# Performance work log

Measured on AMD Instinct MI355X. Metric: run time of the kernel, lower is better.

Reference implementation:

```python
import jax, jax.numpy as jnp
import numpy as np

B, L, D, H = 8, 1024, 512, 8
HD = D // H            # head_dim = 64
MAX_SEQ = 1024         # max_sequence_len
TEMP = 1.0


def setup_inputs() -> dict:
    key = jax.random.key(0)
    ks = jax.random.split(key, 9)
    w = lambda k, shape: jax.random.normal(k, shape, jnp.float32) * 0.02
    return {
        "x_q": jax.random.normal(ks[0], (B, L, D), jnp.float32),
        "x_k": jax.random.normal(ks[1], (B, L, D), jnp.float32),
        "x_v": jax.random.normal(ks[2], (B, L, D), jnp.float32),
        # causal mask: 1 where future (masked), 0 elsewhere; added as mask * -1e9
        "mask": jnp.triu(jnp.ones((L, L), jnp.float32), k=1),
        "Wq": w(ks[3], (D, D)), "bq": jnp.zeros((D,), jnp.float32),
        "Wk": w(ks[4], (D, D)), "bk": jnp.zeros((D,), jnp.float32),
        "Wv": w(ks[5], (D, D)), "bv": jnp.zeros((D,), jnp.float32),
        "Wo": w(ks[6], (D, D)), "bo": jnp.zeros((D,), jnp.float32),
        "rel_emb": w(ks[7], (MAX_SEQ, HD)),
    }


def _heads(x, W, b):
    # Dense + split heads: [B,L,D] -> [B,H,L,HD]
    y = x @ W + b
    Bx, Lx, _ = x.shape
    return y.reshape(Bx, Lx, H, HD).transpose(0, 2, 1, 3)


def reference(x_q, x_k, x_v, mask, Wq, bq, Wk, bk, Wv, bv, Wo, bo, rel_emb):
    Bx, Lq, Dx = x_q.shape
    Lk = x_k.shape[1]
    q = _heads(x_q, Wq, bq)   # [B,H,Lq,HD]
    k = _heads(x_k, Wk, bk)   # [B,H,Lk,HD]
    v = _heads(x_v, Wv, bv)   # [B,H,Lk,HD]

    scores = jnp.einsum('bhld,bhmd->bhlm', q, k)  # [B,H,Lq,Lk]

    # relative-position scores (Music Transformer skew trick)
    start = max(0, MAX_SEQ - Lq)
    E = rel_emb[start:]                              # [M,HD], M == Lq
    M = E.shape[0]
    rel = jnp.einsum('bhld,md->bhlm', q, E)          # [B,H,Lq,M]
    rel_mask = jnp.flip(jnp.tril(jnp.ones((Lq, M), jnp.float32)), axis=1)
    rel = rel * rel_mask
    # skew: pad one col on left, reshape swapping last two dims, drop first row
    padded = jnp.pad(rel, ((0, 0), (0, 0), (0, 0), (1, 0)))       # [B,H,Lq,M+1]
    skewed = padded.reshape(Bx, H, M + 1, Lq)[:, :, 1:, :]        # [B,H,M,Lq]
    skewed = skewed[:, :, :, :Lk]                                 # key_len <= query_len

    logits = (scores + skewed) / (jnp.sqrt(jnp.float32(HD)) * TEMP)
    logits = logits + mask * (-1e9)
    attn = jax.nn.softmax(logits, axis=-1)                        # [B,H,Lq,Lk]

    out = jnp.einsum('bhlm,bhmd->bhld', attn, v)                  # [B,H,Lq,HD]
    out = out.transpose(0, 2, 1, 3).reshape(Bx, Lq, Dx)
    out = out @ Wo + bo
    return out, attn
```

## Files before the change

### kernel.cpp

```cpp
#include <hip/hip_runtime.h>

typedef unsigned short u16;
typedef short bf8 __attribute__((ext_vector_type(8)));
typedef float f32x4 __attribute__((ext_vector_type(4)));

#define Bc 8
#define Hc 8
#define Lc 1024
#define Dc 512
#define HDc 64

__device__ __forceinline__ u16 f2bf(float f) {
    unsigned int x; __builtin_memcpy(&x, &f, 4);
    x = x + 0x7fffu + ((x >> 16) & 1u);
    return (u16)(x >> 16);
}
union S8 { bf8 v; u16 s[8]; };

__global__ __launch_bounds__(256) void relcvt(const float* __restrict__ src,
                                              u16* __restrict__ dst) {
    const int idx = blockIdx.x * 256 + threadIdx.x;
    const float4 v = *(const float4*)(src + (size_t)idx * 4);
    ushort4 o; o.x = f2bf(v.x); o.y = f2bf(v.y); o.z = f2bf(v.z); o.w = f2bf(v.w);
    *(ushort4*)(dst + (size_t)idx * 4) = o;
}

__global__ __launch_bounds__(256) void wtrans(
    const float* __restrict__ w0, const float* __restrict__ w1,
    const float* __restrict__ w2, const float* __restrict__ w3,
    u16* __restrict__ o0, u16* __restrict__ o1,
    u16* __restrict__ o2, u16* __restrict__ o3)
{
    const float* W; u16* O;
    switch (blockIdx.z) {
        case 0: W = w0; O = o0; break;
        case 1: W = w1; O = o1; break;
        case 2: W = w2; O = o2; break;
        default: W = w3; O = o3; break;
    }
    __shared__ float tile[64][65];
    const int t = threadIdx.x;
    const int k0 = blockIdx.x * 64, n0 = blockIdx.y * 64;
#pragma unroll
    for (int s = 0; s < 4; ++s) {
        const int idx = s * 256 + t;
        const int r = idx >> 4, c = (idx & 15) * 4;
        const float4 v = *(const float4*)(W + (size_t)(k0 + r) * Dc + n0 + c);
        tile[r][c] = v.x; tile[r][c + 1] = v.y; tile[r][c + 2] = v.z; tile[r][c + 3] = v.w;
    }
    __syncthreads();
#pragma unroll
    for (int s = 0; s < 2; ++s) {
        const int idx = s * 256 + t;
        const int rn = idx >> 3, ck = (idx & 7) * 8;
        S8 o;
#pragma unroll
        for (int u = 0; u < 8; ++u) o.s[u] = f2bf(tile[ck + u][rn]);
        *(bf8*)(O + (size_t)(n0 + rn) * Dc + k0 + ck) = o.v;
    }
}

__global__ __launch_bounds__(256) void gemm_mfma(
    const void* __restrict__ A, const u16* __restrict__ WT,
    const float* __restrict__ bias, void* __restrict__ Y,
    int aF32, int mode)
{
    __shared__ u16 As[2][64][72];
    __shared__ u16 Bs[2][64][72];

    const int wgid = blockIdx.x;
    const int xcd = wgid & 7, rr = wgid >> 3;
    const int mt = xcd + 8 * (rr >> 3), ntile = rr & 7;
    const int m0 = mt * 64, n0 = ntile * 64;

    const int t = threadIdx.x;
    const int w = t >> 6, lane = t & 63, quad = lane >> 4, l15 = lane & 15;
    const int ra = t >> 2, ca = (t & 3) * 16;

    f32x4 acc[4] = {};

    {
        S8 o0, o1;
        if (aF32) {
            const float* ap = (const float*)A + (size_t)(m0 + ra) * Dc + ca;
            const float4 v0 = *(const float4*)ap,       v1 = *(const float4*)(ap + 4);
            const float4 v2 = *(const float4*)(ap + 8), v3 = *(const float4*)(ap + 12);
            o0.s[0] = f2bf(v0.x); o0.s[1] = f2bf(v0.y); o0.s[2] = f2bf(v0.z); o0.s[3] = f2bf(v0.w);
            o0.s[4] = f2bf(v1.x); o0.s[5] = f2bf(v1.y); o0.s[6] = f2bf(v1.z); o0.s[7] = f2bf(v1.w);
            o1.s[0] = f2bf(v2.x); o1.s[1] = f2bf(v2.y); o1.s[2] = f2bf(v2.z); o1.s[3] = f2bf(v2.w);
            o1.s[4] = f2bf(v3.x); o1.s[5] = f2bf(v3.y); o1.s[6] = f2bf(v3.z); o1.s[7] = f2bf(v3.w);
        } else {
            const u16* ap = (const u16*)A + (size_t)(m0 + ra) * Dc + ca;
            o0.v = *(const bf8*)ap; o1.v = *(const bf8*)(ap + 8);
        }
        *(bf8*)&As[0][ra][ca] = o0.v; *(bf8*)&As[0][ra][ca + 8] = o1.v;
        const u16* bp = WT + (size_t)(n0 + ra) * Dc + ca;
        *(bf8*)&Bs[0][ra][ca] = *(const bf8*)bp;
        *(bf8*)&Bs[0][ra][ca + 8] = *(const bf8*)(bp + 8);
    }

    int cur = 0;
    for (int k0 = 0; k0 < Dc; k0 += 64) {
        __syncthreads();
        const bool pf = (k0 + 64 < Dc);
        float4 v0, v1, v2, v3; bf8 an0 = {}, an1 = {}, bn0 = {}, bn1 = {};
        if (pf) {
            const int kn = k0 + 64;
            if (aF32) {
                const float* ap = (const float*)A + (size_t)(m0 + ra) * Dc + kn + ca;
                v0 = *(const float4*)ap;       v1 = *(const float4*)(ap + 4);
                v2 = *(const float4*)(ap + 8); v3 = *(const float4*)(ap + 12);
            } else {
                const u16* ap = (const u16*)A + (size_t)(m0 + ra) * Dc + kn + ca;
                an0 = *(const bf8*)ap; an1 = *(const bf8*)(ap + 8);
            }
            const u16* bp = WT + (size_t)(n0 + ra) * Dc + kn + ca;
            bn0 = *(const bf8*)bp; bn1 = *(const bf8*)(bp + 8);
        }

#pragma unroll
        for (int ks = 0; ks < 2; ++ks) {
            const bf8 a = *(const bf8*)&As[cur][w * 16 + l15][ks * 32 + quad * 8];
#pragma unroll
            for (int nt = 0; nt < 4; ++nt) {
                const bf8 b = *(const bf8*)&Bs[cur][nt * 16 + l15][ks * 32 + quad * 8];
                acc[nt] = __builtin_amdgcn_mfma_f32_16x16x32_bf16(a, b, acc[nt], 0, 0, 0);
            }
        }

        if (pf) {
            S8 o0, o1;
            if (aF32) {
                o0.s[0] = f2bf(v0.x); o0.s[1] = f2bf(v0.y); o0.s[2] = f2bf(v0.z); o0.s[3] = f2bf(v0.w);
                o0.s[4] = f2bf(v1.x); o0.s[5] = f2bf(v1.y); o0.s[6] = f2bf(v1.z); o0.s[7] = f2bf(v1.w);
                o1.s[0] = f2bf(v2.x); o1.s[1] = f2bf(v2.y); o1.s[2] = f2bf(v2.z); o1.s[3] = f2bf(v2.w);
                o1.s[4] = f2bf(v3.x); o1.s[5] = f2bf(v3.y); o1.s[6] = f2bf(v3.z); o1.s[7] = f2bf(v3.w);
            } else { o0.v = an0; o1.v = an1; }
            *(bf8*)&As[cur ^ 1][ra][ca] = o0.v; *(bf8*)&As[cur ^ 1][ra][ca + 8] = o1.v;
            *(bf8*)&Bs[cur ^ 1][ra][ca] = bn0;  *(bf8*)&Bs[cur ^ 1][ra][ca + 8] = bn1;
            cur ^= 1;
        }
    }

#pragma unroll
    for (int nt = 0; nt < 4; ++nt) {
        const int n = n0 + nt * 16 + l15;
        const float bv = bias[n];
#pragma unroll
        for (int reg = 0; reg < 4; ++reg) {
            const int m = m0 + w * 16 + quad * 4 + reg;
            const float val = acc[nt][reg] + bv;
            if (mode == 0) {
                __builtin_nontemporal_store(val, (float*)Y + (size_t)m * Dc + n);
            } else {
                const int b = m >> 10, l = m & 1023;
                const int h = n >> 6, hd = n & 63;
                ((u16*)Y)[(((size_t)(b * Hc + h)) * Lc + l) * HDc + hd] = f2bf(val);
            }
        }
    }
}

__global__ __launch_bounds__(256) void attn_mfma(
    const u16* __restrict__ q, const u16* __restrict__ k,
    const u16* __restrict__ v, const u16* __restrict__ rel,
    float* __restrict__ attn, u16* __restrict__ ows)
{
    __shared__ u16 kps[2][64][72];
    __shared__ u16 vst[64][72];
    __shared__ u16 es[3][64][72];
    __shared__ float rs[64][96];
    __shared__ float ls[64];

    const int bh = blockIdx.x;
    const int px = blockIdx.y;
    const int t = threadIdx.x;
    const int w = t >> 6, lane = t & 63, quad = lane >> 4, l15 = lane & 15;
    const size_t qb = ((size_t)bh << 10);
    const int sr = t >> 3, scb = (t & 7) * 8;

    for (int seg = 0; seg < 2; ++seg) {
        const int it = seg ? (15 - px) : px;
        const int i0 = it * 64;
        const int mb0 = 960 - i0;

        __syncthreads();
        if (t < 64) ls[t] = 0.f;

        bf8 aq[2];
#pragma unroll
        for (int ks = 0; ks < 2; ++ks)
            aq[ks] = *(const bf8*)(q + (qb + i0 + w * 16 + l15) * HDc + ks * 32 + quad * 8);

        {
            const bf8 k0r = *(const bf8*)(k + (qb + sr) * HDc + scb);
            const bf8 k1r = *(const bf8*)(k + (qb + 32 + sr) * HDc + scb);
            *(bf8*)&kps[0][sr][scb] = k0r;
            *(bf8*)&kps[0][32 + sr][scb] = k1r;
#pragma unroll
            for (int s = 0; s < 4; ++s) {
                const int idx = s * 256 + t;
                const int r = idx >> 3, cb = (idx & 7) * 8;
                int row = mb0 + r; row = row > 1023 ? 1023 : row;
                *(bf8*)&es[r >> 6][r & 63][cb] = *(const bf8*)(rel + (size_t)row * HDc + cb);
            }
        }
        int cur = 0, h0 = 0, h1 = 1, h2 = 2;
        for (int jt = 0; jt <= it; ++jt) {
            const int j0 = jt * 64;
            __syncthreads();
            const bool pf = (jt < it);
            bf8 kn0 = {}, kn1 = {};
            if (pf) {
                kn0 = *(const bf8*)(k + (qb + j0 + 64 + sr) * HDc + scb);
                kn1 = *(const bf8*)(k + (qb + j0 + 96 + sr) * HDc + scb);
                const int rb = mb0 + j0 + 128;
#pragma unroll
                for (int s = 0; s < 2; ++s) {
                    const int idx = s * 256 + t;
                    const int r = idx >> 3, cb = (idx & 7) * 8;
                    int row = rb + r; row = row > 1023 ? 1023 : row;
                    *(bf8*)&es[h2][r][cb] = *(const bf8*)(rel + (size_t)row * HDc + cb);
                }
            }

            f32x4 aS[4] = {}; f32x4 aR[5] = {};
#pragma unroll
            for (int ks = 0; ks < 2; ++ks) {
                const bf8 a = aq[ks];
#pragma unroll
                for (int nt = 0; nt < 4; ++nt) {
                    const bf8 b = *(const bf8*)&kps[cur][nt * 16 + l15][ks * 32 + quad * 8];
                    aS[nt] = __builtin_amdgcn_mfma_f32_16x16x32_bf16(a, b, aS[nt], 0, 0, 0);
                }
#pragma unroll
                for (int nt = 0; nt < 5; ++nt) {
                    const int rr = 3 - w + nt;
                    const bf8 b = *(const bf8*)&es[(rr >= 4) ? h1 : h0]
                                                 [(rr & 3) * 16 + l15][ks * 32 + quad * 8];
                    aR[nt] = __builtin_amdgcn_mfma_f32_16x16x32_bf16(a, b, aR[nt], 0, 0, 0);
                }
            }
#pragma unroll
            for (int nt = 0; nt < 5; ++nt)
#pragma unroll
                for (int reg = 0; reg < 4; ++reg)
                    rs[w * 16 + quad * 4 + reg][nt * 16 + l15] = aR[nt][reg];

            float psum[4] = {0.f, 0.f, 0.f, 0.f};
#pragma unroll
            for (int nt = 0; nt < 4; ++nt) {
#pragma unroll
                for (int reg = 0; reg < 4; ++reg) {
                    const int Rl = w * 16 + quad * 4 + reg;
                    const int cp = 15 - quad * 4 - reg + nt * 16 + l15;
                    const float sc = (aS[nt][reg] + rs[Rl][cp]) * 0.125f;
                    const bool valid = (j0 + nt * 16 + l15) <= (i0 + Rl);
                    psum[reg] += valid ? __expf(sc) : 0.f;
                }
            }
#pragma unroll
            for (int m = 1; m < 16; m <<= 1)
#pragma unroll
                for (int reg = 0; reg < 4; ++reg) psum[reg] += __shfl_xor(psum[reg], m, 64);
            if (l15 == 0) {
#pragma unroll
                for (int reg = 0; reg < 4; ++reg) ls[w * 16 + quad * 4 + reg] += psum[reg];
            }
            if (pf) {
                *(bf8*)&kps[cur ^ 1][sr][scb] = kn0;
                *(bf8*)&kps[cur ^ 1][32 + sr][scb] = kn1;
                cur ^= 1;
            }
            { const int tp = h0; h0 = h1; h1 = h2; h2 = tp; }
        }

        __syncthreads();
        if (t < 64) ls[t] = 1.f / ls[t];

        f32x4 acc[4] = {};

        {
            const bf8 k0r = *(const bf8*)(k + (qb + sr) * HDc + scb);
            const bf8 k1r = *(const bf8*)(k + (qb + 32 + sr) * HDc + scb);
            S8 v0; v0.v = *(const bf8*)(v + (qb + sr) * HDc + scb);
            S8 v1; v1.v = *(const bf8*)(v + (qb + 32 + sr) * HDc + scb);
            *(bf8*)&kps[0][sr][scb] = k0r;
            *(bf8*)&kps[0][32 + sr][scb] = k1r;
            const int cp0 = (sr & 7) + 8 * (((sr >> 3) + (scb >> 3)) & 7);
            const int cp1 = (sr & 7) + 8 * ((4 + (sr >> 3) + (scb >> 3)) & 7);
#pragma unroll
            for (int u = 0; u < 8; ++u) vst[scb + u][cp0] = v0.s[u];
#pragma unroll
            for (int u = 0; u < 8; ++u) vst[scb + u][cp1] = v1.s[u];
#pragma unroll
            for (int s = 0; s < 4; ++s) {
                const int idx = s * 256 + t;
                const int r = idx >> 3, cb = (idx & 7) * 8;
                int row = mb0 + r; row = row > 1023 ? 1023 : row;
                *(bf8*)&es[r >> 6][r & 63][cb] = *(const bf8*)(rel + (size_t)row * HDc + cb);
            }
        }
        cur = 0; h0 = 0; h1 = 1; h2 = 2;
        for (int jt = 0; jt <= it; ++jt) {
            const int j0 = jt * 64;
            __syncthreads();
            const bool pf = (jt < it);
            bf8 kn0 = {}, kn1 = {}, vn0 = {}, vn1 = {};
            if (pf) {
                kn0 = *(const bf8*)(k + (qb + j0 + 64 + sr) * HDc + scb);
                kn1 = *(const bf8*)(k + (qb + j0 + 96 + sr) * HDc + scb);
                vn0 = *(const bf8*)(v + (qb + j0 + 64 + sr) * HDc + scb);
                vn1 = *(const bf8*)(v + (qb + j0 + 96 + sr) * HDc + scb);
                const int rb = mb0 + j0 + 128;
#pragma unroll
                for (int s = 0; s < 2; ++s) {
                    const int idx = s * 256 + t;
                    const int r = idx >> 3, cb = (idx & 7) * 8;
                    int row = rb + r; row = row > 1023 ? 1023 : row;
                    *(bf8*)&es[h2][r][cb] = *(const bf8*)(rel + (size_t)row * HDc + cb);
                }
            }

            f32x4 aS[4] = {}; f32x4 aR[5] = {};
#pragma unroll
            for (int ks = 0; ks < 2; ++ks) {
                const bf8 a = aq[ks];
#pragma unroll
                for (int nt = 0; nt < 4; ++nt) {
                    const bf8 b = *(const bf8*)&kps[cur][nt * 16 + l15][ks * 32 + quad * 8];
                    aS[nt] = __builtin_amdgcn_mfma_f32_16x16x32_bf16(a, b, aS[nt], 0, 0, 0);
                }
#pragma unroll
                for (int nt = 0; nt < 5; ++nt) {
                    const int rr = 3 - w + nt;
                    const bf8 b = *(const bf8*)&es[(rr >= 4) ? h1 : h0]
                                                 [(rr & 3) * 16 + l15][ks * 32 + quad * 8];
                    aR[nt] = __builtin_amdgcn_mfma_f32_16x16x32_bf16(a, b, aR[nt], 0, 0, 0);
                }
            }
#pragma unroll
            for (int nt = 0; nt < 5; ++nt)
#pragma unroll
                for (int reg = 0; reg < 4; ++reg)
                    rs[w * 16 + quad * 4 + reg][nt * 16 + l15] = aR[nt][reg];

            float pvv[4][4];
#pragma unroll
            for (int nt = 0; nt < 4; ++nt) {
#pragma unroll
                for (int reg = 0; reg < 4; ++reg) {
                    const int Rl = w * 16 + quad * 4 + reg;
                    const int cp = 15 - quad * 4 - reg + nt * 16 + l15;
                    const float sc = (aS[nt][reg] + rs[Rl][cp]) * 0.125f;
                    const bool valid = (j0 + nt * 16 + l15) <= (i0 + Rl);
                    pvv[nt][reg] = valid ? __expf(sc) * ls[Rl] : 0.f;
                }
            }
            asm volatile("" ::: "memory");
#pragma unroll
            for (int nt = 0; nt < 4; ++nt) {
#pragma unroll
                for (int reg = 0; reg < 4; ++reg) {
                    const int Rl = w * 16 + quad * 4 + reg;
                    ((u16*)&rs[Rl][0])[nt * 16 + l15] = f2bf(pvv[nt][reg]);
                    rs[Rl][32 + nt * 16 + l15] = pvv[nt][reg];
                }
            }

#pragma unroll
            for (int ks = 0; ks < 2; ++ks) {
                const bf8 pa = *(const bf8*)((const u16*)&rs[w * 16 + l15][0] + ks * 32 + quad * 8);
#pragma unroll
                for (int nt = 0; nt < 4; ++nt) {
                    const int d = nt * 16 + l15;
                    const bf8 vb = *(const bf8*)&vst[d][8 * (((ks * 4 + quad) + (d >> 3)) & 7)];
                    acc[nt] = __builtin_amdgcn_mfma_f32_16x16x32_bf16(pa, vb, acc[nt], 0, 0, 0);
                }
            }

            if (pf) {
                *(bf8*)&kps[cur ^ 1][sr][scb] = kn0;
                *(bf8*)&kps[cur ^ 1][32 + sr][scb] = kn1;
                cur ^= 1;
            }

            __syncthreads();
            const int trow = t >> 4, tcol = (t & 15) * 4;
#pragma unroll
            for (int s = 0; s < 4; ++s) {
                const f32x4 p4 = *(const f32x4*)&rs[trow + 16 * s][32 + tcol];
                __builtin_nontemporal_store(p4,
                    (f32x4*)(attn + ((size_t)bh * Lc + i0 + trow + 16 * s) * Lc + j0 + tcol));
            }
            if (pf) {
                S8 a0; a0.v = vn0; S8 a1; a1.v = vn1;
                const int cp0 = (sr & 7) + 8 * (((sr >> 3) + (scb >> 3)) & 7);
                const int cp1 = (sr & 7) + 8 * ((4 + (sr >> 3) + (scb >> 3)) & 7);
#pragma unroll
                for (int u = 0; u < 8; ++u) vst[scb + u][cp0] = a0.s[u];
#pragma unroll
                for (int u = 0; u < 8; ++u) vst[scb + u][cp1] = a1.s[u];
            }
            { const int tp = h0; h0 = h1; h1 = h2; h2 = tp; }
        }

        const int bb = bh >> 3, hh = bh & 7;
#pragma unroll
        for (int nt = 0; nt < 4; ++nt)
#pragma unroll
            for (int reg = 0; reg < 4; ++reg)
                ows[((size_t)(bb * Lc + i0 + w * 16 + quad * 4 + reg)) * Dc + hh * HDc + nt * 16 + l15]
                    = f2bf(acc[nt][reg]);

        const int jend = (it + 1) * 64;
        if (jend + t * 4 < Lc) {
            const f32x4 z = {0.f, 0.f, 0.f, 0.f};
            for (int r = 0; r < 64; ++r)
                __builtin_nontemporal_store(z,
                    (f32x4*)(attn + ((size_t)bh * Lc + i0 + r) * Lc + jend + t * 4));
        }
    }
}

extern "C" void kernel_launch(void* const* d_in, const int* in_sizes, int n_in,
                              void* d_out, int out_size, void* d_ws, size_t ws_size,
                              hipStream_t stream)
{
    const float* x_q = (const float*)d_in[0];
    const float* x_k = (const float*)d_in[1];
    const float* x_v = (const float*)d_in[2];
    const float* Wq = (const float*)d_in[4];
    const float* bq = (const float*)d_in[5];
    const float* Wk = (const float*)d_in[6];
    const float* bk = (const float*)d_in[7];
    const float* Wv = (const float*)d_in[8];
    const float* bv = (const float*)d_in[9];
    const float* Wo = (const float*)d_in[10];
    const float* bo = (const float*)d_in[11];
    const float* rel = (const float*)d_in[12];

    float* out  = (float*)d_out;
    float* attn = out + (size_t)Bc * Lc * Dc;

    u16* relbf = (u16*)d_ws;
    u16* wqT = relbf + (size_t)1024 * 64;
    u16* wkT = wqT + (size_t)Dc * Dc;
    u16* wvT = wkT + (size_t)Dc * Dc;
    u16* woT = wvT + (size_t)Dc * Dc;
    u16* qbf = woT + (size_t)Dc * Dc;
    u16* kbf = qbf + (size_t)Bc * Lc * Dc;
    u16* vbf = kbf + (size_t)Bc * Lc * Dc;
    u16* owsbf = vbf + (size_t)Bc * Lc * Dc;

    relcvt<<<64, 256, 0, stream>>>(rel, relbf);
    wtrans<<<dim3(8, 8, 4), 256, 0, stream>>>(Wq, Wk, Wv, Wo, wqT, wkT, wvT, woT);

    gemm_mfma<<<1024, 256, 0, stream>>>(x_q, wqT, bq, qbf, 1, 1);
    gemm_mfma<<<1024, 256, 0, stream>>>(x_k, wkT, bk, kbf, 1, 1);
    gemm_mfma<<<1024, 256, 0, stream>>>(x_v, wvT, bv, vbf, 1, 1);

    attn_mfma<<<dim3(64, 8), 256, 0, stream>>>(qbf, kbf, vbf, relbf, attn, owsbf);

    gemm_mfma<<<1024, 256, 0, stream>>>(owsbf, woT, bo, out, 0, 0);
}
```

Baseline: 451.5 us.

## Fuse QKV GEMMs into one launch and give each attention block one query tile

The three Q/K/V projection GEMMs become a single launch with blockIdx.y choosing the operand set. The attention kernel now runs one query tile per block over a 64x16 grid, with the heaviest tiles scheduled first, replacing the paired light/heavy tile scheme. Shared memory shrinks: single-buffered K, double-buffered rel-embedding tiles loaded through registers, and a skew-aligned rs buffer so the softmax reads unshifted columns. Row sums now stay in registers instead of going through shared atomic-style updates. This doubles the attention grid for better occupancy and load spreading, at the cost of losing the light/heavy pairing that balanced the causal work per block.

```diff
diff --git a/kernel.cpp b/kernel.cpp
--- a/kernel.cpp
+++ b/kernel.cpp
@@ -60,7 +60,7 @@
     }
 }
 
-__global__ __launch_bounds__(256) void gemm_mfma(
+__device__ __forceinline__ void gemm_core(
     const void* __restrict__ A, const u16* __restrict__ WT,
     const float* __restrict__ bias, void* __restrict__ Y,
     int aF32, int mode)
@@ -161,265 +161,270 @@
     }
 }
 
+__global__ __launch_bounds__(256) void gemm_mfma(
+    const void* __restrict__ A, const u16* __restrict__ WT,
+    const float* __restrict__ bias, void* __restrict__ Y,
+    int aF32, int mode)
+{
+    gemm_core(A, WT, bias, Y, aF32, mode);
+}
+
+__global__ __launch_bounds__(256) void gemm_qkv(
+    const float* __restrict__ xq, const float* __restrict__ xk, const float* __restrict__ xv,
+    const u16* __restrict__ wq, const u16* __restrict__ wk, const u16* __restrict__ wv,
+    const float* __restrict__ bq, const float* __restrict__ bk, const float* __restrict__ bv,
+    u16* __restrict__ yq, u16* __restrict__ yk, u16* __restrict__ yv)
+{
+    const float* A; const u16* W; const float* bb; u16* y;
+    switch (blockIdx.y) {
+        case 0:  A = xq; W = wq; bb = bq; y = yq; break;
+        case 1:  A = xk; W = wk; bb = bk; y = yk; break;
+        default: A = xv; W = wv; bb = bv; y = yv; break;
+    }
+    gemm_core(A, W, bb, y, 1, 1);
+}
+
 __global__ __launch_bounds__(256) void attn_mfma(
     const u16* __restrict__ q, const u16* __restrict__ k,
     const u16* __restrict__ v, const u16* __restrict__ rel,
     float* __restrict__ attn, u16* __restrict__ ows)
 {
-    __shared__ u16 kps[2][64][72];
+    __shared__ u16 kps[64][72];
     __shared__ u16 vst[64][72];
-    __shared__ u16 es[3][64][72];
-    __shared__ float rs[64][96];
-    __shared__ float ls[64];
+    __shared__ u16 es[2][64][72];
+    __shared__ float rs[64][68];
 
     const int bh = blockIdx.x;
-    const int px = blockIdx.y;
+    const int it = 15 - (int)blockIdx.y;
+    const int i0 = it * 64;
+    const int mb0 = 960 - i0;
     const int t = threadIdx.x;
     const int w = t >> 6, lane = t & 63, quad = lane >> 4, l15 = lane & 15;
     const size_t qb = ((size_t)bh << 10);
     const int sr = t >> 3, scb = (t & 7) * 8;
-
-    for (int seg = 0; seg < 2; ++seg) {
-        const int it = seg ? (15 - px) : px;
-        const int i0 = it * 64;
-        const int mb0 = 960 - i0;
-
+    const int rb4 = quad * 4;
+    const int Rw = w * 16;
+
+    bf8 aq[2];
+#pragma unroll
+    for (int ks = 0; ks < 2; ++ks)
+        aq[ks] = *(const bf8*)(q + (qb + i0 + Rw + l15) * HDc + ks * 32 + quad * 8);
+
+    float lsum[4] = {0.f, 0.f, 0.f, 0.f};
+
+    {
+        *(bf8*)&kps[sr][scb] = *(const bf8*)(k + (qb + sr) * HDc + scb);
+        *(bf8*)&kps[32 + sr][scb] = *(const bf8*)(k + (qb + 32 + sr) * HDc + scb);
+#pragma unroll
+        for (int s = 0; s < 4; ++s) {
+            const int idx = s * 256 + t;
+            const int r = idx >> 3, cb = (idx & 7) * 8;
+            int row = mb0 + r; row = row > 1023 ? 1023 : row;
+            *(bf8*)&es[r >> 6][r & 63][cb] = *(const bf8*)(rel + (size_t)row * HDc + cb);
+        }
+    }
+    for (int jt = 0; jt <= it; ++jt) {
+        const int j0 = jt * 64;
+        const int lo = jt & 1;
         __syncthreads();
-        if (t < 64) ls[t] = 0.f;
-
-        bf8 aq[2];
-#pragma unroll
-        for (int ks = 0; ks < 2; ++ks)
-            aq[ks] = *(const bf8*)(q + (qb + i0 + w * 16 + l15) * HDc + ks * 32 + quad * 8);
-
+        const bool pf = (jt < it);
+        bf8 kn0 = {}, kn1 = {}, en0 = {}, en1 = {};
+        if (pf) {
+            kn0 = *(const bf8*)(k + (qb + j0 + 64 + sr) * HDc + scb);
+            kn1 = *(const bf8*)(k + (qb + j0 + 96 + sr) * HDc + scb);
+            const int rbr = mb0 + j0 + 128;
+            int r0 = rbr + sr;      r0 = r0 > 1023 ? 1023 : r0;
+            int r1 = rbr + 32 + sr; r1 = r1 > 1023 ? 1023 : r1;
+            en0 = *(const bf8*)(rel + (size_t)r0 * HDc + scb);
+            en1 = *(const bf8*)(rel + (size_t)r1 * HDc + scb);
+        }
+
+        f32x4 aS[4] = {}; f32x4 aR[5] = {};
+#pragma unroll
+        for (int ks = 0; ks < 2; ++ks) {
+            const bf8 a = aq[ks];
+#pragma unroll
+            for (int nt = 0; nt < 4; ++nt) {
+                const bf8 b = *(const bf8*)&kps[nt * 16 + l15][ks * 32 + quad * 8];
+                aS[nt] = __builtin_amdgcn_mfma_f32_16x16x32_bf16(a, b, aS[nt], 0, 0, 0);
+            }
+#pragma unroll
+            for (int nt = 0; nt < 5; ++nt) {
+                const int rr = 3 - w + nt;
+                const bf8 b = *(const bf8*)&es[lo ^ (rr >> 2)][(rr & 3) * 16 + l15][ks * 32 + quad * 8];
+                aR[nt] = __builtin_amdgcn_mfma_f32_16x16x32_bf16(a, b, aR[nt], 0, 0, 0);
+            }
+        }
+#pragma unroll
+        for (int nt = 0; nt < 5; ++nt)
+#pragma unroll
+            for (int reg = 0; reg < 4; ++reg) {
+                const int jv = nt * 16 + l15 - 15 + rb4 + reg;
+                if ((unsigned)jv < 64u) rs[Rw + rb4 + reg][jv] = aR[nt][reg];
+            }
+        __syncthreads();
+        if (pf) {
+            *(bf8*)&kps[sr][scb] = kn0;
+            *(bf8*)&kps[32 + sr][scb] = kn1;
+            *(bf8*)&es[lo][sr][scb] = en0;
+            *(bf8*)&es[lo][32 + sr][scb] = en1;
+        }
+
+        float psum[4] = {0.f, 0.f, 0.f, 0.f};
+#pragma unroll
+        for (int nt = 0; nt < 4; ++nt) {
+#pragma unroll
+            for (int reg = 0; reg < 4; ++reg) {
+                const int Rl = Rw + rb4 + reg;
+                const int J = nt * 16 + l15;
+                const float sc = (aS[nt][reg] + rs[Rl][J]) * 0.125f;
+                const bool valid = (j0 + J) <= (i0 + Rl);
+                psum[reg] += valid ? __expf(sc) : 0.f;
+            }
+        }
+#pragma unroll
+        for (int m = 1; m < 16; m <<= 1)
+#pragma unroll
+            for (int reg = 0; reg < 4; ++reg) psum[reg] += __shfl_xor(psum[reg], m, 64);
+#pragma unroll
+        for (int reg = 0; reg < 4; ++reg) lsum[reg] += psum[reg];
+    }
+
+    __syncthreads();
+    float ils[4];
+#pragma unroll
+    for (int reg = 0; reg < 4; ++reg) ils[reg] = 1.f / lsum[reg];
+
+    f32x4 acc[4] = {};
+
+    {
+        *(bf8*)&kps[sr][scb] = *(const bf8*)(k + (qb + sr) * HDc + scb);
+        *(bf8*)&kps[32 + sr][scb] = *(const bf8*)(k + (qb + 32 + sr) * HDc + scb);
+        S8 v0; v0.v = *(const bf8*)(v + (qb + sr) * HDc + scb);
+        S8 v1; v1.v = *(const bf8*)(v + (qb + 32 + sr) * HDc + scb);
+        const int cp0 = (sr & 7) + 8 * (((sr >> 3) + (scb >> 3)) & 7);
+        const int cp1 = (sr & 7) + 8 * ((4 + (sr >> 3) + (scb >> 3)) & 7);
+#pragma unroll
+        for (int u = 0; u < 8; ++u) vst[scb + u][cp0] = v0.s[u];
+#pragma unroll
+        for (int u = 0; u < 8; ++u) vst[scb + u][cp1] = v1.s[u];
+#pragma unroll
+        for (int s = 0; s < 4; ++s) {
+            const int idx = s * 256 + t;
+            const int r = idx >> 3, cb = (idx & 7) * 8;
+            int row = mb0 + r; row = row > 1023 ? 1023 : row;
+            *(bf8*)&es[r >> 6][r & 63][cb] = *(const bf8*)(rel + (size_t)row * HDc + cb);
+        }
+    }
+    for (int jt = 0; jt <= it; ++jt) {
+        const int j0 = jt * 64;
+        const int lo = jt & 1;
+        __syncthreads();
+        const bool pf = (jt < it);
+        bf8 kn0 = {}, kn1 = {}, vn0 = {}, vn1 = {}, en0 = {}, en1 = {};
+        if (pf) {
+            kn0 = *(const bf8*)(k + (qb + j0 + 64 + sr) * HDc + scb);
+            kn1 = *(const bf8*)(k + (qb + j0 + 96 + sr) * HDc + scb);
+            vn0 = *(const bf8*)(v + (qb + j0 + 64 + sr) * HDc + scb);
+            vn1 = *(const bf8*)(v + (qb + j0 + 96 + sr) * HDc + scb);
+            const int rbr = mb0 + j0 + 128;
+            int r0 = rbr + sr;      r0 = r0 > 1023 ? 1023 : r0;
+            int r1 = rbr + 32 + sr; r1 = r1 > 1023 ? 1023 : r1;
+            en0 = *(const bf8*)(rel + (size_t)r0 * HDc + scb);
+            en1 = *(const bf8*)(rel + (size_t)r1 * HDc + scb);
+        }
+
+        f32x4 aS[4] = {}; f32x4 aR[5] = {};
+#pragma unroll
+        for (int ks = 0; ks < 2; ++ks) {
+            const bf8 a = aq[ks];
+#pragma unroll
+            for (int nt = 0; nt < 4; ++nt) {
+                const bf8 b = *(const bf8*)&kps[nt * 16 + l15][ks * 32 + quad * 8];
+                aS[nt] = __builtin_amdgcn_mfma_f32_16x16x32_bf16(a, b, aS[nt], 0, 0, 0);
+            }
+#pragma unroll
+            for (int nt = 0; nt < 5; ++nt) {
+                const int rr = 3 - w + nt;
+                const bf8 b = *(const bf8*)&es[lo ^ (rr >> 2)][(rr & 3) * 16 + l15][ks * 32 + quad * 8];
+                aR[nt] = __builtin_amdgcn_mfma_f32_16x16x32_bf16(a, b, aR[nt], 0, 0, 0);
+            }
+        }
+#pragma unroll
+        for (int nt = 0; nt < 5; ++nt)
+#pragma unroll
+            for (int reg = 0; reg < 4; ++reg) {
+                const int jv = nt * 16 + l15 - 15 + rb4 + reg;
+                if ((unsigned)jv < 64u) rs[Rw + rb4 + reg][jv] = aR[nt][reg];
+            }
+
+#pragma unroll
+        for (int nt = 0; nt < 4; ++nt) {
+#pragma unroll
+            for (int reg = 0; reg < 4; ++reg) {
+                const int Rl = Rw + rb4 + reg;
+                const int J = nt * 16 + l15;
+                const float sc = (aS[nt][reg] + rs[Rl][J]) * 0.125f;
+                const bool valid = (j0 + J) <= (i0 + Rl);
+                const float p = valid ? __expf(sc) * ils[reg] : 0.f;
+                rs[Rl][J] = p;
+            }
+        }
+
+#pragma unroll
+        for (int ks = 0; ks < 2; ++ks) {
+            const f32x4 pa0 = *(const f32x4*)&rs[Rw + l15][ks * 32 + quad * 8];
+            const f32x4 pa1 = *(const f32x4*)&rs[Rw + l15][ks * 32 + quad * 8 + 4];
+            S8 pk;
+#pragma unroll
+            for (int u = 0; u < 4; ++u) { pk.s[u] = f2bf(pa0[u]); pk.s[4 + u] = f2bf(pa1[u]); }
+#pragma unroll
+            for (int nt = 0; nt < 4; ++nt) {
+                const int d = nt * 16 + l15;
+                const bf8 vb = *(const bf8*)&vst[d][8 * (((ks * 4 + quad) + (d >> 3)) & 7)];
+                acc[nt] = __builtin_amdgcn_mfma_f32_16x16x32_bf16(pk.v, vb, acc[nt], 0, 0, 0);
+            }
+        }
+
+        __syncthreads();
         {
-            const bf8 k0r = *(const bf8*)(k + (qb + sr) * HDc + scb);
-            const bf8 k1r = *(const bf8*)(k + (qb + 32 + sr) * HDc + scb);
-            *(bf8*)&kps[0][sr][scb] = k0r;
-            *(bf8*)&kps[0][32 + sr][scb] = k1r;
+            const int trow = t >> 4, tcol = (t & 15) * 4;
 #pragma unroll
             for (int s = 0; s < 4; ++s) {
-                const int idx = s * 256 + t;
-                const int r = idx >> 3, cb = (idx & 7) * 8;
-                int row = mb0 + r; row = row > 1023 ? 1023 : row;
-                *(bf8*)&es[r >> 6][r & 63][cb] = *(const bf8*)(rel + (size_t)row * HDc + cb);
-            }
-        }
-        int cur = 0, h0 = 0, h1 = 1, h2 = 2;
-        for (int jt = 0; jt <= it; ++jt) {
-            const int j0 = jt * 64;
-            __syncthreads();
-            const bool pf = (jt < it);
-            bf8 kn0 = {}, kn1 = {};
-            if (pf) {
-                kn0 = *(const bf8*)(k + (qb + j0 + 64 + sr) * HDc + scb);
-                kn1 = *(const bf8*)(k + (qb + j0 + 96 + sr) * HDc + scb);
-                const int rb = mb0 + j0 + 128;
-#pragma unroll
-                for (int s = 0; s < 2; ++s) {
-                    const int idx = s * 256 + t;
-                    const int r = idx >> 3, cb = (idx & 7) * 8;
-                    int row = rb + r; row = row > 1023 ? 1023 : row;
-                    *(bf8*)&es[h2][r][cb] = *(const bf8*)(rel + (size_t)row * HDc + cb);
-                }
-            }
-
-            f32x4 aS[4] = {}; f32x4 aR[5] = {};
-#pragma unroll
-            for (int ks = 0; ks < 2; ++ks) {
-                const bf8 a = aq[ks];
-#pragma unroll
-                for (int nt = 0; nt < 4; ++nt) {
-                    const bf8 b = *(const bf8*)&kps[cur][nt * 16 + l15][ks * 32 + quad * 8];
-                    aS[nt] = __builtin_amdgcn_mfma_f32_16x16x32_bf16(a, b, aS[nt], 0, 0, 0);
-                }
-#pragma unroll
-                for (int nt = 0; nt < 5; ++nt) {
-                    const int rr = 3 - w + nt;
-                    const bf8 b = *(const bf8*)&es[(rr >= 4) ? h1 : h0]
-                                                 [(rr & 3) * 16 + l15][ks * 32 + quad * 8];
-                    aR[nt] = __builtin_amdgcn_mfma_f32_16x16x32_bf16(a, b, aR[nt], 0, 0, 0);
-                }
-            }
-#pragma unroll
-            for (int nt = 0; nt < 5; ++nt)
-#pragma unroll
-                for (int reg = 0; reg < 4; ++reg)
-                    rs[w * 16 + quad * 4 + reg][nt * 16 + l15] = aR[nt][reg];
-
-            float psum[4] = {0.f, 0.f, 0.f, 0.f};
-#pragma unroll
-            for (int nt = 0; nt < 4; ++nt) {
-#pragma unroll
-                for (int reg = 0; reg < 4; ++reg) {
-                    const int Rl = w * 16 + quad * 4 + reg;
-                    const int cp = 15 - quad * 4 - reg + nt * 16 + l15;
-                    const float sc = (aS[nt][reg] + rs[Rl][cp]) * 0.125f;
-                    const bool valid = (j0 + nt * 16 + l15) <= (i0 + Rl);
-                    psum[reg] += valid ? __expf(sc) : 0.f;
-                }
-            }
-#pragma unroll
-            for (int m = 1; m < 16; m <<= 1)
-#pragma unroll
-                for (int reg = 0; reg < 4; ++reg) psum[reg] += __shfl_xor(psum[reg], m, 64);
-            if (l15 == 0) {
-#pragma unroll
-                for (int reg = 0; reg < 4; ++reg) ls[w * 16 + quad * 4 + reg] += psum[reg];
-            }
-            if (pf) {
-                *(bf8*)&kps[cur ^ 1][sr][scb] = kn0;
-                *(bf8*)&kps[cur ^ 1][32 + sr][scb] = kn1;
-                cur ^= 1;
-            }
-            { const int tp = h0; h0 = h1; h1 = h2; h2 = tp; }
-        }
-
-        __syncthreads();
-        if (t < 64) ls[t] = 1.f / ls[t];
-
-        f32x4 acc[4] = {};
-
-        {
-            const bf8 k0r = *(const bf8*)(k + (qb + sr) * HDc + scb);
-            const bf8 k1r = *(const bf8*)(k + (qb + 32 + sr) * HDc + scb);
-            S8 v0; v0.v = *(const bf8*)(v + (qb + sr) * HDc + scb);
-            S8 v1; v1.v = *(const bf8*)(v + (qb + 32 + sr) * HDc + scb);
-            *(bf8*)&kps[0][sr][scb] = k0r;
-            *(bf8*)&kps[0][32 + sr][scb] = k1r;
+                const f32x4 p4 = *(const f32x4*)&rs[trow + 16 * s][tcol];
+                __builtin_nontemporal_store(p4,
+                    (f32x4*)(attn + ((size_t)bh * Lc + i0 + trow + 16 * s) * Lc + j0 + tcol));
+            }
+        }
+        if (pf) {
+            *(bf8*)&kps[sr][scb] = kn0;
+            *(bf8*)&kps[32 + sr][scb] = kn1;
+            S8 a0; a0.v = vn0; S8 a1; a1.v = vn1;
             const int cp0 = (sr & 7) + 8 * (((sr >> 3) + (scb >> 3)) & 7);
             const int cp1 = (sr & 7) + 8 * ((4 + (sr >> 3) + (scb >> 3)) & 7);
 #pragma unroll
-            for (int u = 0; u < 8; ++u) vst[scb + u][cp0] = v0.s[u];
-#pragma unroll
-            for (int u = 0; u < 8; ++u) vst[scb + u][cp1] = v1.s[u];
-#pragma unroll
-            for (int s = 0; s < 4; ++s) {
-                const int idx = s * 256 + t;
-                const int r = idx >> 3, cb = (idx & 7) * 8;
-                int row = mb0 + r; row = row > 1023 ? 1023 : row;
-                *(bf8*)&es[r >> 6][r & 63][cb] = *(const bf8*)(rel + (size_t)row * HDc + cb);
-            }
-        }
-        cur = 0; h0 = 0; h1 = 1; h2 = 2;
-        for (int jt = 0; jt <= it; ++jt) {
-            const int j0 = jt * 64;
-            __syncthreads();
-            const bool pf = (jt < it);
-            bf8 kn0 = {}, kn1 = {}, vn0 = {}, vn1 = {};
-            if (pf) {
-                kn0 = *(const bf8*)(k + (qb + j0 + 64 + sr) * HDc + scb);
-                kn1 = *(const bf8*)(k + (qb + j0 + 96 + sr) * HDc + scb);
-                vn0 = *(const bf8*)(v + (qb + j0 + 64 + sr) * HDc + scb);
-                vn1 = *(const bf8*)(v + (qb + j0 + 96 + sr) * HDc + scb);
-                const int rb = mb0 + j0 + 128;
-#pragma unroll
-                for (int s = 0; s < 2; ++s) {
-                    const int idx = s * 256 + t;
-                    const int r = idx >> 3, cb = (idx & 7) * 8;
-                    int row = rb + r; row = row > 1023 ? 1023 : row;
-                    *(bf8*)&es[h2][r][cb] = *(const bf8*)(rel + (size_t)row * HDc + cb);
-                }
-            }
-
-            f32x4 aS[4] = {}; f32x4 aR[5] = {};
-#pragma unroll
-            for (int ks = 0; ks < 2; ++ks) {
-                const bf8 a = aq[ks];
-#pragma unroll
-                for (int nt = 0; nt < 4; ++nt) {
-                    const bf8 b = *(const bf8*)&kps[cur][nt * 16 + l15][ks * 32 + quad * 8];
-                    aS[nt] = __builtin_amdgcn_mfma_f32_16x16x32_bf16(a, b, aS[nt], 0, 0, 0);
-                }
-#pragma unroll
-                for (int nt = 0; nt < 5; ++nt) {
-                    const int rr = 3 - w + nt;
-                    const bf8 b = *(const bf8*)&es[(rr >= 4) ? h1 : h0]
-                                                 [(rr & 3) * 16 + l15][ks * 32 + quad * 8];
-                    aR[nt] = __builtin_amdgcn_mfma_f32_16x16x32_bf16(a, b, aR[nt], 0, 0, 0);
-                }
-            }
-#pragma unroll
-            for (int nt = 0; nt < 5; ++nt)
-#pragma unroll
-                for (int reg = 0; reg < 4; ++reg)
-                    rs[w * 16 + quad * 4 + reg][nt * 16 + l15] = aR[nt][reg];
-
-            float pvv[4][4];
-#pragma unroll
-            for (int nt = 0; nt < 4; ++nt) {
-#pragma unroll
-                for (int reg = 0; reg < 4; ++reg) {
-                    const int Rl = w * 16 + quad * 4 + reg;
-                    const int cp = 15 - quad * 4 - reg + nt * 16 + l15;
-                    const float sc = (aS[nt][reg] + rs[Rl][cp]) * 0.125f;
-                    const bool valid = (j0 + nt * 16 + l15) <= (i0 + Rl);
-                    pvv[nt][reg] = valid ? __expf(sc) * ls[Rl] : 0.f;
-                }
-            }
-            asm volatile("" ::: "memory");
-#pragma unroll
-            for (int nt = 0; nt < 4; ++nt) {
-#pragma unroll
-                for (int reg = 0; reg < 4; ++reg) {
-                    const int Rl = w * 16 + quad * 4 + reg;
-                    ((u16*)&rs[Rl][0])[nt * 16 + l15] = f2bf(pvv[nt][reg]);
-                    rs[Rl][32 + nt * 16 + l15] = pvv[nt][reg];
-                }
-            }
-
-#pragma unroll
-            for (int ks = 0; ks < 2; ++ks) {
-                const bf8 pa = *(const bf8*)((const u16*)&rs[w * 16 + l15][0] + ks * 32 + quad * 8);
-#pragma unroll
-                for (int nt = 0; nt < 4; ++nt) {
-                    const int d = nt * 16 + l15;
-                    const bf8 vb = *(const bf8*)&vst[d][8 * (((ks * 4 + quad) + (d >> 3)) & 7)];
-                    acc[nt] = __builtin_amdgcn_mfma_f32_16x16x32_bf16(pa, vb, acc[nt], 0, 0, 0);
-                }
-            }
-
-            if (pf) {
-                *(bf8*)&kps[cur ^ 1][sr][scb] = kn0;
-                *(bf8*)&kps[cur ^ 1][32 + sr][scb] = kn1;
-                cur ^= 1;
-            }
-
-            __syncthreads();
-            const int trow = t >> 4, tcol = (t & 15) * 4;
-#pragma unroll
-            for (int s = 0; s < 4; ++s) {
-                const f32x4 p4 = *(const f32x4*)&rs[trow + 16 * s][32 + tcol];
-                __builtin_nontemporal_store(p4,
-                    (f32x4*)(attn + ((size_t)bh * Lc + i0 + trow + 16 * s) * Lc + j0 + tcol));
-            }
-            if (pf) {
-                S8 a0; a0.v = vn0; S8 a1; a1.v = vn1;
-                const int cp0 = (sr & 7) + 8 * (((sr >> 3) + (scb >> 3)) & 7);
-                const int cp1 = (sr & 7) + 8 * ((4 + (sr >> 3) + (scb >> 3)) & 7);
-#pragma unroll
-                for (int u = 0; u < 8; ++u) vst[scb + u][cp0] = a0.s[u];
-#pragma unroll
-                for (int u = 0; u < 8; ++u) vst[scb + u][cp1] = a1.s[u];
-            }
-            { const int tp = h0; h0 = h1; h1 = h2; h2 = tp; }
-        }
-
-        const int bb = bh >> 3, hh = bh & 7;
-#pragma unroll
-        for (int nt = 0; nt < 4; ++nt)
-#pragma unroll
-            for (int reg = 0; reg < 4; ++reg)
-                ows[((size_t)(bb * Lc + i0 + w * 16 + quad * 4 + reg)) * Dc + hh * HDc + nt * 16 + l15]
-                    = f2bf(acc[nt][reg]);
-
-        const int jend = (it + 1) * 64;
-        if (jend + t * 4 < Lc) {
-            const f32x4 z = {0.f, 0.f, 0.f, 0.f};
-            for (int r = 0; r < 64; ++r)
-                __builtin_nontemporal_store(z,
-                    (f32x4*)(attn + ((size_t)bh * Lc + i0 + r) * Lc + jend + t * 4));
-        }
+            for (int u = 0; u < 8; ++u) vst[scb + u][cp0] = a0.s[u];
+#pragma unroll
+            for (int u = 0; u < 8; ++u) vst[scb + u][cp1] = a1.s[u];
+            *(bf8*)&es[lo][sr][scb] = en0;
+            *(bf8*)&es[lo][32 + sr][scb] = en1;
+        }
+    }
+
+    const int bb = bh >> 3, hh = bh & 7;
+#pragma unroll
+    for (int nt = 0; nt < 4; ++nt)
+#pragma unroll
+        for (int reg = 0; reg < 4; ++reg)
+            ows[((size_t)(bb * Lc + i0 + Rw + rb4 + reg)) * Dc + hh * HDc + nt * 16 + l15]
+                = f2bf(acc[nt][reg]);
+
+    const int jend = (it + 1) * 64;
+    if (jend + t * 4 < Lc) {
+        const f32x4 z = {0.f, 0.f, 0.f, 0.f};
+        for (int r = 0; r < 64; ++r)
+            __builtin_nontemporal_store(z,
+                (f32x4*)(attn + ((size_t)bh * Lc + i0 + r) * Lc + jend + t * 4));
     }
 }
 
@@ -456,11 +461,10 @@
     relcvt<<<64, 256, 0, stream>>>(rel, relbf);
     wtrans<<<dim3(8, 8, 4), 256, 0, stream>>>(Wq, Wk, Wv, Wo, wqT, wkT, wvT, woT);
 
-    gemm_mfma<<<1024, 256, 0, stream>>>(x_q, wqT, bq, qbf, 1, 1);
-    gemm_mfma<<<1024, 256, 0, stream>>>(x_k, wkT, bk, kbf, 1, 1);
-    gemm_mfma<<<1024, 256, 0, stream>>>(x_v, wvT, bv, vbf, 1, 1);
-
-    attn_mfma<<<dim3(64, 8), 256, 0, stream>>>(qbf, kbf, vbf, relbf, attn, owsbf);
+    gemm_qkv<<<dim3(1024, 3), 256, 0, stream>>>(x_q, x_k, x_v, wqT, wkT, wvT,
+                                                bq, bk, bv, qbf, kbf, vbf);
+
+    attn_mfma<<<dim3(64, 16), 256, 0, stream>>>(qbf, kbf, vbf, relbf, attn, owsbf);
 
     gemm_mfma<<<1024, 256, 0, stream>>>(owsbf, woT, bo, out, 0, 0);
 }
```

Result: no change. 456.2 us (+1.0%).
